# Kernel tuning notes

Hardware: AMD Instinct MI355X
Metric: run time of the kernel (lower is better)

The kernel has to match this reference:

```python
import jax, jax.numpy as jnp
import numpy as np

NUM_HEADS = 16
DIM_HEAD = 64
SCALE = DIM_HEAD ** -0.5


def setup_inputs() -> dict:
    key = jax.random.key(0)
    k1, k2, k3 = jax.random.split(key, 3)
    b, s, h = 2, 2048, 1024
    x = jax.random.normal(k1, (b, s, h), dtype=jnp.float32)
    w_qkv = jax.random.normal(k2, (3 * h, h), dtype=jnp.float32) * (h ** -0.5)
    w_out = jax.random.normal(k3, (h, h), dtype=jnp.float32) * (h ** -0.5)
    b_out = jnp.zeros((h,), dtype=jnp.float32)
    return {"x": x, "w_qkv": w_qkv, "w_out": w_out, "b_out": b_out}


def reference(x, w_qkv, w_out, b_out):
    b, s, hid = x.shape
    # qkv projection (no bias): [b, s, 3*hid]
    qkv = jnp.einsum('bsh,oh->bso', x, w_qkv)
    # split order in original rearrange is (qkv, heads, dim_head)
    qkv = qkv.reshape(b, s, 3, NUM_HEADS, DIM_HEAD)
    q = jnp.transpose(qkv[:, :, 0], (0, 2, 1, 3))  # [b, H, s, d]
    k = jnp.transpose(qkv[:, :, 1], (0, 2, 1, 3))
    v = jnp.transpose(qkv[:, :, 2], (0, 2, 1, 3))
    # naive attention: full [b, H, s, s] score matrix, as in the source
    att = jnp.einsum('bhxd,bhyd->bhxy', q, k) * SCALE
    att = jax.nn.softmax(att, axis=-1)
    out = jnp.einsum('bhxy,bhyd->bhxd', att, v)  # [b, H, s, d]
    out = jnp.transpose(out, (0, 2, 1, 3)).reshape(b, s, NUM_HEADS * DIM_HEAD)
    return jnp.einsum('bsi,oi->bso', out, w_out) + b_out
```

## Files before the change

### kernel.cpp

```cpp
#include <hip/hip_runtime.h>
#include <hip/hip_bf16.h>

#define B_ 2
#define S_ 2048
#define HID 1024
#define NH 16
#define DH 64
#define QKV_N (3*HID)
#define M_ROWS (B_*S_)
#define SCALE 0.125f

typedef __attribute__((ext_vector_type(8))) short short8;
typedef __attribute__((ext_vector_type(4))) short short4v;
typedef __attribute__((ext_vector_type(4))) float floatx4;

__device__ __forceinline__ short8 load8(const __hip_bfloat16* p) {
    return *(const short8*)p;
}

#define ASYNC16(gptr, lptr) \
    __builtin_amdgcn_global_load_lds((const __attribute__((address_space(1))) void*)(gptr), \
                                     (__attribute__((address_space(3))) void*)(lptr), 16, 0, 0)

__global__ __launch_bounds__(256) void cvt_f32_bf16(
    const float* __restrict__ in, __hip_bfloat16* __restrict__ out, int n)
{
    int i = (blockIdx.x * 256 + threadIdx.x) * 4;
    if (i + 3 < n) {
        float4 v = *(const float4*)(in + i);
        __hip_bfloat16 h[4];
        h[0] = __float2bfloat16(v.x);
        h[1] = __float2bfloat16(v.y);
        h[2] = __float2bfloat16(v.z);
        h[3] = __float2bfloat16(v.w);
        *(short4v*)(out + i) = *(short4v*)h;
    }
}

#define BK 32
template<int MODE>
__global__ __launch_bounds__(256) void gemm_bt_kernel(
    const __hip_bfloat16* __restrict__ A,
    const __hip_bfloat16* __restrict__ Bw,
    const float* __restrict__ biasf,
    __hip_bfloat16* __restrict__ C,
    float* __restrict__ Cf,
    __hip_bfloat16* __restrict__ VT,
    int Mdim, int Ndim, int Kdim)
{
    __shared__ alignas(16) __hip_bfloat16 As[128 * BK];
    __shared__ alignas(16) __hip_bfloat16 Bs[128 * BK];

    const int tid  = threadIdx.x;
    const int wave = tid >> 6;
    const int lane = tid & 63;
    const int q = lane >> 4;
    const int r = lane & 15;
    const int m_blk = blockIdx.y * 128;
    const int n_blk = blockIdx.x * 128;
    const int wm = (wave >> 1) * 64;
    const int wn = (wave & 1) * 64;

    const int srow = tid >> 2;
    const int skc  = tid & 3;
    const __hip_bfloat16* gA = A + (size_t)(m_blk + srow) * Kdim + skc * 8;
    const __hip_bfloat16* gB = Bw + (size_t)(n_blk + srow) * Kdim + skc * 8;
    char* ldsA0 = (char*)As + (size_t)tid * 16;
    char* ldsA1 = ldsA0 + 4096;
    char* ldsB0 = (char*)Bs + (size_t)tid * 16;
    char* ldsB1 = ldsB0 + 4096;
    const size_t rs64 = (size_t)64 * Kdim;

    floatx4 acc[4][4];
#pragma unroll
    for (int i = 0; i < 4; i++)
#pragma unroll
        for (int j = 0; j < 4; j++) acc[i][j] = (floatx4){0.f, 0.f, 0.f, 0.f};

    for (int kt = 0; kt < Kdim; kt += BK) {
        __syncthreads();
        ASYNC16(gA + kt,        ldsA0);
        ASYNC16(gA + rs64 + kt, ldsA1);
        ASYNC16(gB + kt,        ldsB0);
        ASYNC16(gB + rs64 + kt, ldsB1);
        __builtin_amdgcn_s_waitcnt(0);
        __syncthreads();

        short8 a[4], b[4];
#pragma unroll
        for (int i = 0; i < 4; i++) a[i] = *(const short8*)&As[(wm + i * 16 + r) * BK + q * 8];
#pragma unroll
        for (int j = 0; j < 4; j++) b[j] = *(const short8*)&Bs[(wn + j * 16 + r) * BK + q * 8];
#pragma unroll
        for (int i = 0; i < 4; i++)
#pragma unroll
            for (int j = 0; j < 4; j++)
                acc[i][j] = __builtin_amdgcn_mfma_f32_16x16x32_bf16(a[i], b[j], acc[i][j], 0, 0, 0);
    }

#pragma unroll
    for (int i = 0; i < 4; i++) {
#pragma unroll
        for (int j = 0; j < 4; j++) {
#pragma unroll
            for (int reg = 0; reg < 4; reg++) {
                int m = m_blk + wm + i * 16 + q * 4 + reg;
                int n = n_blk + wn + j * 16 + r;
                float v = acc[i][j][reg];
                if (MODE == 2) {
                    Cf[(size_t)m * Ndim + n] = v + biasf[n];
                } else {
                    __hip_bfloat16 hv = __float2bfloat16(v);
                    if (n < 2 * HID) {
                        C[(size_t)m * QKV_N + n] = hv;
                    } else {
                        int dfull = n - 2 * HID;
                        int bidx = m >> 11;
                        int s = m & (S_ - 1);
                        int c = s & 63;
                        int sp = (s & ~63) | ((c & 15) << 2) | ((c >> 4) & 3);
                        VT[((size_t)bidx * HID + dfull) * S_ + sp] = hv;
                    }
                }
            }
        }
    }
}

#define KT 64
#define PPAD 72
#define SCALE2 0.18033688f
#define FM2 23.083120f

__global__ __launch_bounds__(256, 2) void flash_kernel(
    const __hip_bfloat16* __restrict__ qkv,
    const __hip_bfloat16* __restrict__ VTp,
    __hip_bfloat16* __restrict__ O)
{
    __shared__ alignas(16) __hip_bfloat16 lds_k[2][64 * 64];
    __shared__ alignas(16) __hip_bfloat16 lds_v[2][64 * 64];
    __shared__ alignas(16) __hip_bfloat16 lds_p[4][32 * PPAD];

    const int tid  = threadIdx.x;
    const int wave = tid >> 6;
    const int lane = tid & 63;
    const int q = lane >> 4;
    const int r = lane & 15;
    const int bh = blockIdx.x;
    const int b  = bh >> 4;
    const int h  = bh & 15;
    const int s0 = blockIdx.y * 128 + wave * 32;

    const __hip_bfloat16* Qbase = qkv + (size_t)b * S_ * QKV_N + h * DH;
    const __hip_bfloat16* Kbase = Qbase + HID;
    const __hip_bfloat16* Vbase = VTp + ((size_t)b * HID + h * DH) * S_;

    const int srow = wave * 16 + (lane >> 3);
    const int cglob = (lane & 7) ^ ((lane >> 3) & 7);
    const __hip_bfloat16* gK = Kbase + (size_t)srow * QKV_N + cglob * 8;
    const __hip_bfloat16* gV = Vbase + (size_t)srow * S_ + cglob * 8;
    const int ldso = srow * 64 + (lane & 7) * 8;

    short8 a_q[2][2];
#pragma unroll
    for (int rt = 0; rt < 2; rt++)
#pragma unroll
        for (int kh = 0; kh < 2; kh++)
            a_q[rt][kh] = load8(Qbase + (size_t)(s0 + rt * 16 + r) * QKV_N + kh * 32 + q * 8);

    floatx4 o_acc[2][4];
    floatx4 l_acc[2];
#pragma unroll
    for (int rt = 0; rt < 2; rt++) {
        l_acc[rt] = (floatx4){0.f, 0.f, 0.f, 0.f};
#pragma unroll
        for (int nb = 0; nb < 4; nb++) o_acc[rt][nb] = (floatx4){0.f, 0.f, 0.f, 0.f};
    }

    short8 ones;
#pragma unroll
    for (int i = 0; i < 8; i++) ones[i] = (short)0x3F80;

    __hip_bfloat16* Pw = &lds_p[wave][0];

    ASYNC16(gK,                         &lds_k[0][ldso]);
    ASYNC16(gK + (size_t)8 * QKV_N,     &lds_k[0][ldso + 8 * 64]);
    ASYNC16(gV,                         &lds_v[0][ldso]);
    ASYNC16(gV + (size_t)8 * S_,        &lds_v[0][ldso + 8 * 64]);

    for (int it = 0; it < S_ / KT; it++) {
        const int cur = it & 1, nxt = cur ^ 1;
        const int kt = it * KT;
        __builtin_amdgcn_s_waitcnt(0);
        __syncthreads();
        if (it + 1 < S_ / KT) {
            ASYNC16(gK + (size_t)(kt + KT) * QKV_N,     &lds_k[nxt][ldso]);
            ASYNC16(gK + (size_t)(kt + KT + 8) * QKV_N, &lds_k[nxt][ldso + 8 * 64]);
            ASYNC16(gV + (kt + KT),                     &lds_v[nxt][ldso]);
            ASYNC16(gV + (size_t)8 * S_ + (kt + KT),    &lds_v[nxt][ldso + 8 * 64]);
        }

        short8 bk[4][2];
#pragma unroll
        for (int ct = 0; ct < 4; ct++)
#pragma unroll
            for (int kh = 0; kh < 2; kh++)
                bk[ct][kh] = *(const short8*)&lds_k[cur][(ct * 16 + r) * 64 + ((kh * 4 + q) ^ (r & 7)) * 8];

#pragma unroll
        for (int rt = 0; rt < 2; rt++) {
            floatx4 sc[4];
#pragma unroll
            for (int ct = 0; ct < 4; ct++) {
                floatx4 z = (floatx4){0.f, 0.f, 0.f, 0.f};
                z = __builtin_amdgcn_mfma_f32_16x16x32_bf16(a_q[rt][0], bk[ct][0], z, 0, 0, 0);
                z = __builtin_amdgcn_mfma_f32_16x16x32_bf16(a_q[rt][1], bk[ct][1], z, 0, 0, 0);
                sc[ct] = z;
            }
#pragma unroll
            for (int reg = 0; reg < 4; reg++) {
                __hip_bfloat16 pk[4];
#pragma unroll
                for (int ct = 0; ct < 4; ct++)
                    pk[ct] = __float2bfloat16(exp2f(fmaf(sc[ct][reg], SCALE2, -FM2)));
                *(short4v*)&Pw[(rt * 16 + q * 4 + reg) * PPAD + 4 * r] = *(const short4v*)pk;
            }
        }
        __builtin_amdgcn_s_waitcnt(0xc07f);

        short8 vb[4][2];
#pragma unroll
        for (int nb = 0; nb < 4; nb++)
#pragma unroll
            for (int kh = 0; kh < 2; kh++)
                vb[nb][kh] = *(const short8*)&lds_v[cur][(nb * 16 + r) * 64 + ((kh * 4 + q) ^ (r & 7)) * 8];

#pragma unroll
        for (int rt = 0; rt < 2; rt++) {
            short8 pa0 = *(const short8*)&Pw[(rt * 16 + r) * PPAD + q * 8];
            short8 pa1 = *(const short8*)&Pw[(rt * 16 + r) * PPAD + 32 + q * 8];
            l_acc[rt] = __builtin_amdgcn_mfma_f32_16x16x32_bf16(pa0, ones, l_acc[rt], 0, 0, 0);
            l_acc[rt] = __builtin_amdgcn_mfma_f32_16x16x32_bf16(pa1, ones, l_acc[rt], 0, 0, 0);
#pragma unroll
            for (int nb = 0; nb < 4; nb++) {
                o_acc[rt][nb] = __builtin_amdgcn_mfma_f32_16x16x32_bf16(pa0, vb[nb][0], o_acc[rt][nb], 0, 0, 0);
                o_acc[rt][nb] = __builtin_amdgcn_mfma_f32_16x16x32_bf16(pa1, vb[nb][1], o_acc[rt][nb], 0, 0, 0);
            }
        }
    }

#pragma unroll
    for (int rt = 0; rt < 2; rt++) {
#pragma unroll
        for (int reg = 0; reg < 4; reg++) {
            float inv = 1.f / l_acc[rt][reg];
            int srow2 = s0 + rt * 16 + q * 4 + reg;
            __hip_bfloat16* Orow = O + ((size_t)b * S_ + srow2) * HID + h * DH;
#pragma unroll
            for (int nb = 0; nb < 4; nb++)
                Orow[nb * 16 + r] = __float2bfloat16(o_acc[rt][nb][reg] * inv);
        }
    }
}

extern "C" void kernel_launch(void* const* d_in, const int* in_sizes, int n_in,
                              void* d_out, int out_size, void* d_ws, size_t ws_size,
                              hipStream_t stream) {
    const float* x_f     = (const float*)d_in[0];
    const float* w_qkv_f = (const float*)d_in[1];
    const float* w_out_f = (const float*)d_in[2];
    const float* b_out_f = (const float*)d_in[3];
    float* out = (float*)d_out;

    __hip_bfloat16* xb      = (__hip_bfloat16*)d_ws;
    __hip_bfloat16* wqkvb   = xb    + (size_t)M_ROWS * HID;
    __hip_bfloat16* woutb   = wqkvb + (size_t)QKV_N * HID;
    __hip_bfloat16* qkv_ws  = woutb + (size_t)HID * HID;
    __hip_bfloat16* vt_ws   = qkv_ws + (size_t)M_ROWS * QKV_N;
    __hip_bfloat16* attn_ws = vt_ws + (size_t)B_ * HID * S_;

    dim3 blk(256);
    {
        int n;
        n = M_ROWS * HID; cvt_f32_bf16<<<dim3(n / 1024), blk, 0, stream>>>(x_f, xb, n);
        n = QKV_N * HID;  cvt_f32_bf16<<<dim3(n / 1024), blk, 0, stream>>>(w_qkv_f, wqkvb, n);
        n = HID * HID;    cvt_f32_bf16<<<dim3(n / 1024), blk, 0, stream>>>(w_out_f, woutb, n);
    }

    gemm_bt_kernel<1><<<dim3(QKV_N / 128, M_ROWS / 128), blk, 0, stream>>>(
        xb, wqkvb, nullptr, qkv_ws, nullptr, vt_ws, M_ROWS, QKV_N, HID);
    flash_kernel<<<dim3(B_ * NH, S_ / 128), dim3(256), 0, stream>>>(qkv_ws, vt_ws, attn_ws);
    gemm_bt_kernel<2><<<dim3(HID / 128, M_ROWS / 128), blk, 0, stream>>>(
        attn_ws, woutb, b_out_f, nullptr, out, nullptr, M_ROWS, HID, HID);
}
```

Measured before the change: 216.0 us.

## Split flash attention keys across wave pairs and widen GEMM K-tile with swizzled LDS

The flash kernel now handles 64 query rows per block instead of 128. Two wave pairs each process half of the key sequence (split-K), and their O and l partial sums are combined through LDS at the end. The grid doubles, occupancy is raised to 3 blocks per CU, and the K/V double-buffered prefetch is dropped in favour of synchronous per-tile loads. Separately, the GEMM K-tile grows from 32 to 64 with an XOR-swizzled LDS layout to cut bank conflicts and halve the barrier count. The risk is losing load/compute overlap in the attention loop.

```diff
diff --git a/kernel.cpp b/kernel.cpp
--- a/kernel.cpp
+++ b/kernel.cpp
@@ -8,7 +8,6 @@
 #define DH 64
 #define QKV_N (3*HID)
 #define M_ROWS (B_*S_)
-#define SCALE 0.125f
 
 typedef __attribute__((ext_vector_type(8))) short short8;
 typedef __attribute__((ext_vector_type(4))) short short4v;
@@ -37,7 +36,7 @@
     }
 }
 
-#define BK 32
+#define BK 64
 template<int MODE>
 __global__ __launch_bounds__(256) void gemm_bt_kernel(
     const __hip_bfloat16* __restrict__ A,
@@ -61,15 +60,12 @@
     const int wm = (wave >> 1) * 64;
     const int wn = (wave & 1) * 64;
 
-    const int srow = tid >> 2;
-    const int skc  = tid & 3;
-    const __hip_bfloat16* gA = A + (size_t)(m_blk + srow) * Kdim + skc * 8;
-    const __hip_bfloat16* gB = Bw + (size_t)(n_blk + srow) * Kdim + skc * 8;
-    char* ldsA0 = (char*)As + (size_t)tid * 16;
-    char* ldsA1 = ldsA0 + 4096;
-    char* ldsB0 = (char*)Bs + (size_t)tid * 16;
-    char* ldsB1 = ldsB0 + 4096;
-    const size_t rs64 = (size_t)64 * Kdim;
+    const int srow = tid >> 3;
+    const int cglob = (tid & 7) ^ ((tid >> 3) & 7);
+    const __hip_bfloat16* gA = A + (size_t)(m_blk + srow) * Kdim + cglob * 8;
+    const __hip_bfloat16* gB = Bw + (size_t)(n_blk + srow) * Kdim + cglob * 8;
+    char* ldsA = (char*)As + (size_t)tid * 16;
+    char* ldsB = (char*)Bs + (size_t)tid * 16;
 
     floatx4 acc[4][4];
 #pragma unroll
@@ -79,23 +75,29 @@
 
     for (int kt = 0; kt < Kdim; kt += BK) {
         __syncthreads();
-        ASYNC16(gA + kt,        ldsA0);
-        ASYNC16(gA + rs64 + kt, ldsA1);
-        ASYNC16(gB + kt,        ldsB0);
-        ASYNC16(gB + rs64 + kt, ldsB1);
+#pragma unroll
+        for (int c = 0; c < 4; c++) {
+            ASYNC16(gA + kt + (size_t)(c * 32) * Kdim, ldsA + c * 4096);
+            ASYNC16(gB + kt + (size_t)(c * 32) * Kdim, ldsB + c * 4096);
+        }
         __builtin_amdgcn_s_waitcnt(0);
         __syncthreads();
 
-        short8 a[4], b[4];
-#pragma unroll
-        for (int i = 0; i < 4; i++) a[i] = *(const short8*)&As[(wm + i * 16 + r) * BK + q * 8];
-#pragma unroll
-        for (int j = 0; j < 4; j++) b[j] = *(const short8*)&Bs[(wn + j * 16 + r) * BK + q * 8];
-#pragma unroll
-        for (int i = 0; i < 4; i++)
+#pragma unroll
+        for (int kh = 0; kh < 2; kh++) {
+            short8 a[4], b[4];
+#pragma unroll
+            for (int i = 0; i < 4; i++)
+                a[i] = *(const short8*)&As[(wm + i * 16 + r) * BK + (((kh * 4 + q) ^ (r & 7)) * 8)];
 #pragma unroll
             for (int j = 0; j < 4; j++)
-                acc[i][j] = __builtin_amdgcn_mfma_f32_16x16x32_bf16(a[i], b[j], acc[i][j], 0, 0, 0);
+                b[j] = *(const short8*)&Bs[(wn + j * 16 + r) * BK + (((kh * 4 + q) ^ (r & 7)) * 8)];
+#pragma unroll
+            for (int i = 0; i < 4; i++)
+#pragma unroll
+                for (int j = 0; j < 4; j++)
+                    acc[i][j] = __builtin_amdgcn_mfma_f32_16x16x32_bf16(a[i], b[j], acc[i][j], 0, 0, 0);
+        }
     }
 
 #pragma unroll
@@ -132,7 +134,7 @@
 #define SCALE2 0.18033688f
 #define FM2 23.083120f
 
-__global__ __launch_bounds__(256, 2) void flash_kernel(
+__global__ __launch_bounds__(256, 3) void flash_kernel(
     const __hip_bfloat16* __restrict__ qkv,
     const __hip_bfloat16* __restrict__ VTp,
     __hip_bfloat16* __restrict__ O)
@@ -146,20 +148,22 @@
     const int lane = tid & 63;
     const int q = lane >> 4;
     const int r = lane & 15;
+    const int p     = wave & 1;
+    const int khid  = wave >> 1;
     const int bh = blockIdx.x;
     const int b  = bh >> 4;
     const int h  = bh & 15;
-    const int s0 = blockIdx.y * 128 + wave * 32;
+    const int s0 = blockIdx.y * 64 + p * 32;
 
     const __hip_bfloat16* Qbase = qkv + (size_t)b * S_ * QKV_N + h * DH;
     const __hip_bfloat16* Kbase = Qbase + HID;
     const __hip_bfloat16* Vbase = VTp + ((size_t)b * HID + h * DH) * S_;
 
-    const int srow = wave * 16 + (lane >> 3);
+    const int sr = p * 32 + (lane >> 3);
     const int cglob = (lane & 7) ^ ((lane >> 3) & 7);
-    const __hip_bfloat16* gK = Kbase + (size_t)srow * QKV_N + cglob * 8;
-    const __hip_bfloat16* gV = Vbase + (size_t)srow * S_ + cglob * 8;
-    const int ldso = srow * 64 + (lane & 7) * 8;
+    const __hip_bfloat16* gK = Kbase + (size_t)(khid * 1024 + sr) * QKV_N + cglob * 8;
+    const __hip_bfloat16* gV = Vbase + (size_t)sr * S_ + khid * 1024 + cglob * 8;
+    const int ldso = sr * 64 + (lane & 7) * 8;
 
     short8 a_q[2][2];
 #pragma unroll
@@ -183,29 +187,22 @@
 
     __hip_bfloat16* Pw = &lds_p[wave][0];
 
-    ASYNC16(gK,                         &lds_k[0][ldso]);
-    ASYNC16(gK + (size_t)8 * QKV_N,     &lds_k[0][ldso + 8 * 64]);
-    ASYNC16(gV,                         &lds_v[0][ldso]);
-    ASYNC16(gV + (size_t)8 * S_,        &lds_v[0][ldso + 8 * 64]);
-
-    for (int it = 0; it < S_ / KT; it++) {
-        const int cur = it & 1, nxt = cur ^ 1;
-        const int kt = it * KT;
+    for (int it = 0; it < 16; it++) {
+        __syncthreads();
+#pragma unroll
+        for (int c = 0; c < 4; c++) {
+            ASYNC16(gK + (size_t)(it * KT + c * 8) * QKV_N, &lds_k[khid][ldso + c * 512]);
+            ASYNC16(gV + (size_t)(c * 8) * S_ + it * KT,    &lds_v[khid][ldso + c * 512]);
+        }
         __builtin_amdgcn_s_waitcnt(0);
         __syncthreads();
-        if (it + 1 < S_ / KT) {
-            ASYNC16(gK + (size_t)(kt + KT) * QKV_N,     &lds_k[nxt][ldso]);
-            ASYNC16(gK + (size_t)(kt + KT + 8) * QKV_N, &lds_k[nxt][ldso + 8 * 64]);
-            ASYNC16(gV + (kt + KT),                     &lds_v[nxt][ldso]);
-            ASYNC16(gV + (size_t)8 * S_ + (kt + KT),    &lds_v[nxt][ldso + 8 * 64]);
-        }
 
         short8 bk[4][2];
 #pragma unroll
         for (int ct = 0; ct < 4; ct++)
 #pragma unroll
             for (int kh = 0; kh < 2; kh++)
-                bk[ct][kh] = *(const short8*)&lds_k[cur][(ct * 16 + r) * 64 + ((kh * 4 + q) ^ (r & 7)) * 8];
+                bk[ct][kh] = *(const short8*)&lds_k[khid][(ct * 16 + r) * 64 + ((kh * 4 + q) ^ (r & 7)) * 8];
 
 #pragma unroll
         for (int rt = 0; rt < 2; rt++) {
@@ -233,7 +230,7 @@
         for (int nb = 0; nb < 4; nb++)
 #pragma unroll
             for (int kh = 0; kh < 2; kh++)
-                vb[nb][kh] = *(const short8*)&lds_v[cur][(nb * 16 + r) * 64 + ((kh * 4 + q) ^ (r & 7)) * 8];
+                vb[nb][kh] = *(const short8*)&lds_v[khid][(nb * 16 + r) * 64 + ((kh * 4 + q) ^ (r & 7)) * 8];
 
 #pragma unroll
         for (int rt = 0; rt < 2; rt++) {
@@ -249,16 +246,38 @@
         }
     }
 
-#pragma unroll
-    for (int rt = 0; rt < 2; rt++) {
-#pragma unroll
-        for (int reg = 0; reg < 4; reg++) {
-            float inv = 1.f / l_acc[rt][reg];
-            int srow2 = s0 + rt * 16 + q * 4 + reg;
-            __hip_bfloat16* Orow = O + ((size_t)b * S_ + srow2) * HID + h * DH;
+    __syncthreads();
+    float* of = (float*)&lds_k[0][0];
+    float* lf = (float*)&lds_v[0][0];
+    if (khid == 1) {
+#pragma unroll
+        for (int rt = 0; rt < 2; rt++) {
 #pragma unroll
             for (int nb = 0; nb < 4; nb++)
-                Orow[nb * 16 + r] = __float2bfloat16(o_acc[rt][nb][reg] * inv);
+                *(floatx4*)&of[p * 2048 + (rt * 4 + nb) * 256 + lane * 4] = o_acc[rt][nb];
+            *(floatx4*)&lf[p * 512 + rt * 256 + lane * 4] = l_acc[rt];
+        }
+    }
+    __syncthreads();
+    if (khid == 0) {
+#pragma unroll
+        for (int rt = 0; rt < 2; rt++) {
+            l_acc[rt] += *(const floatx4*)&lf[p * 512 + rt * 256 + lane * 4];
+#pragma unroll
+            for (int nb = 0; nb < 4; nb++)
+                o_acc[rt][nb] += *(const floatx4*)&of[p * 2048 + (rt * 4 + nb) * 256 + lane * 4];
+        }
+#pragma unroll
+        for (int rt = 0; rt < 2; rt++) {
+#pragma unroll
+            for (int reg = 0; reg < 4; reg++) {
+                float inv = 1.f / l_acc[rt][reg];
+                int srow2 = s0 + rt * 16 + q * 4 + reg;
+                __hip_bfloat16* Orow = O + ((size_t)b * S_ + srow2) * HID + h * DH;
+#pragma unroll
+                for (int nb = 0; nb < 4; nb++)
+                    Orow[nb * 16 + r] = __float2bfloat16(o_acc[rt][nb][reg] * inv);
+            }
         }
     }
 }
@@ -289,7 +308,7 @@
 
     gemm_bt_kernel<1><<<dim3(QKV_N / 128, M_ROWS / 128), blk, 0, stream>>>(
         xb, wqkvb, nullptr, qkv_ws, nullptr, vt_ws, M_ROWS, QKV_N, HID);
-    flash_kernel<<<dim3(B_ * NH, S_ / 128), dim3(256), 0, stream>>>(qkv_ws, vt_ws, attn_ws);
+    flash_kernel<<<dim3(B_ * NH, S_ / 64), dim3(256), 0, stream>>>(qkv_ws, vt_ws, attn_ws);
     gemm_bt_kernel<2><<<dim3(HID / 128, M_ROWS / 128), blk, 0, stream>>>(
         attn_ws, woutb, b_out_f, nullptr, out, nullptr, M_ROWS, HID, HID);
 }
```

After: 208.2 us. 3.6% less time.
